# Performance work log

Measured on AMD Instinct MI355X. Metric: run time of the kernel, lower is better.

The kernel has to match this reference:

```python
import jax, jax.numpy as jnp
import numpy as np

B = 16384   # batch (agents x parallel envs)
IN = 12     # input_dim
H = 64      # hidden_dim -> 2H = 128
OUT = 25    # output_dim (forced by x[:,0:5]..x[:,20:25] slicing)


def setup_inputs() -> dict:
    key = jax.random.key(0)
    ks = jax.random.split(key, 24)
    n = lambda k, s: jax.random.normal(k, s, dtype=jnp.float32)
    s = 0.1  # scale params to keep SiLU/softmax in a sane range
    return {
        "x": n(ks[0], (B, IN)),
        "na": 4,
        # mlp_in: Linear(IN, 2H) + SiLU
        "W_in": n(ks[1], (2 * H, IN)) * s, "b_in": n(ks[2], (2 * H,)) * s,
        # first attention (2H)
        "Aq4": n(ks[3], (2 * H, 2 * H)) * s, "Bq4": n(ks[4], (2 * H,)) * s,
        "Ak4": n(ks[5], (2 * H, 2 * H)) * s, "Bk4": n(ks[6], (2 * H,)) * s,
        "Av4": n(ks[7], (2 * H, 2 * H)) * s, "Bv4": n(ks[8], (2 * H,)) * s,
        # mlp_hidden_4: Linear(2H, H) + SiLU
        "W_h": n(ks[9], (H, 2 * H)) * s, "b_h": n(ks[10], (H,)) * s,
        # second attention (H)
        "Aq7": n(ks[11], (H, H)) * s, "Bq7": n(ks[12], (H,)) * s,
        "Ak7": n(ks[13], (H, H)) * s, "Bk7": n(ks[14], (H,)) * s,
        "Av7": n(ks[15], (H, H)) * s, "Bv7": n(ks[16], (H,)) * s,
        # mlp_out: Linear(H, OUT) + SiLU
        "W_out": n(ks[17], (OUT, H)) * s, "b_out": n(ks[18], (OUT,)) * s,
    }


def _attn(h, Aq, Bq, Ak, Bk, Av, Bv):
    # h: [B, D]; torch does bmm(A, x^T)+B with x of shape [B,1,D] -> seq-len-1
    # attention, i.e. scores are an outer product q k^T of shape [B, D, D].
    q = jax.nn.silu(h @ Aq.T + Bq)                      # [B, D]
    k = jax.nn.silu(h @ Ak.T + Bk)                      # [B, D]
    v = jax.nn.silu(h @ Av.T + Bv)                      # [B, D]
    a = jax.nn.softmax(q[:, :, None] * k[:, None, :], axis=2)  # [B, D, D]
    return jax.nn.silu(jnp.einsum("bij,bj->bi", a, v))  # [B, D]


def reference(x, na, W_in, b_in, Aq4, Bq4, Ak4, Bk4, Av4, Bv4,
              W_h, b_h, Aq7, Bq7, Ak7, Bk7, Av7, Bv7, W_out, b_out):
    h = jax.nn.silu(x @ W_in.T + b_in)                  # [B, 2H]
    h = _attn(h, Aq4, Bq4, Ak4, Bk4, Av4, Bv4)          # [B, 2H]
    h = jax.nn.silu(h @ W_h.T + b_h)                    # [B, H]
    h = _attn(h, Aq7, Bq7, Ak7, Bk7, Av7, Bv7)          # [B, H]
    y = jax.nn.silu(h @ W_out.T + b_out)                # [B, 25]

    # block-diagonal quadratic-form assembly (l=2, kron with ones(1,2))
    M11 = jnp.sum(y[:, 0:5] ** 2, axis=1)               # [B]
    M12 = jnp.sum(y[:, 5:10] ** 2, axis=1)
    M21 = jnp.sum(y[:, 10:15] ** 2, axis=1)
    M22 = jnp.sum(y[:, 15:20] ** 2, axis=1)
    Mpp = jnp.sum(y[:, 20:25] ** 2, axis=1)             # [B]
    q = y[:, :4]                                        # [B, 4] = [q0,q1,q2,q3]
    # M = [[diag(M11), diag(M12)],[diag(M21), diag(M22)]] (each 2x2 diag)
    quad = (M11 * (q[:, 0] ** 2 + q[:, 1] ** 2)
            + (M12 + M21) * (q[:, 0] * q[:, 2] + q[:, 1] * q[:, 3])
            + M22 * (q[:, 2] ** 2 + q[:, 3] ** 2))
    return (quad + Mpp)[:, None]                        # [B, 1]
```

## Files before the change

### kernel.cpp

```cpp
#include <hip/hip_runtime.h>

#define RPW 4
#define WAVES 4
#define RPB (RPW * WAVES)
#define NM 14

using short8 = __attribute__((ext_vector_type(8))) short;
using f32x4  = __attribute__((ext_vector_type(4))) float;

#define LOG2E 1.4426950408889634f

static __device__ __forceinline__ float ex2(float x) { return __builtin_amdgcn_exp2f(x); }
static __device__ __forceinline__ float rcpf_(float x) { return __builtin_amdgcn_rcpf(x); }
static __device__ __forceinline__ float silu_(float x) {
    return x * rcpf_(1.0f + ex2(-x * LOG2E));
}
static __device__ __forceinline__ unsigned short bfhi(float x) {
    return (unsigned short)(__float_as_uint(x) >> 16);
}
static __device__ __forceinline__ unsigned short bfrn(float x) {
    unsigned u = __float_as_uint(x);
    return (unsigned short)((u + 0x7fffu + ((u >> 16) & 1u)) >> 16);
}
static __device__ __forceinline__ float bf2f(unsigned short h) {
    return __uint_as_float(((unsigned)h) << 16);
}

template <int CTRL>
static __device__ __forceinline__ float dpp_rot(float v) {
    return __uint_as_float(
        __builtin_amdgcn_update_dpp(0u, __float_as_uint(v), CTRL, 0xF, 0xF, true));
}
static __device__ __forceinline__ float rsum16(float v) {
    v += dpp_rot<0x128>(v);
    v += dpp_rot<0x124>(v);
    v += dpp_rot<0x122>(v);
    v += dpp_rot<0x121>(v);
    return v;
}

__constant__ float c_invfact[15] = {
    1.f, 1.f, 0.5f, 1.f/6, 1.f/24, 1.f/120, 1.f/720, 1.f/5040, 1.f/40320,
    1.f/362880, 1.f/3628800, 1.f/39916800, 1.f/479001600,
    1.f/6227020800.f, 1.f/87178291200.f};

template <int O, int I>
__device__ __forceinline__ void tr(const float* __restrict__ s, float* __restrict__ d,
                                   int t0, int stride) {
    for (int idx = t0; idx < O * I; idx += stride) {
        int o = idx / I, in = idx - o * I;
        d[in * O + o] = s[idx];
    }
}

template <int TILES, int KTS, int K>
__device__ __forceinline__ void frag_cvt(const float* __restrict__ A,
                                         unsigned short* __restrict__ dst,
                                         int t0, int stride) {
    const int total = TILES * KTS * 2 * 512;
    for (int idx = t0; idx < total; idx += stride) {
        int e = idx & 7;
        int lane = (idx >> 3) & 63;
        int h = (idx >> 9) & 1;
        int kt = (idx >> 10) % KTS;
        int tile = (idx >> 10) / KTS;
        int row = tile * 16 + (lane & 15);
        int col = kt * 32 + (lane >> 4) * 8 + e;
        float a = A[row * K + col];
        unsigned short hi = bfhi(a);
        dst[idx] = h ? bfhi(a - bf2f(hi)) : hi;
    }
}

__global__ void tweights(const float* __restrict__ s0, const float* __restrict__ s1,
                         const float* __restrict__ s2, const float* __restrict__ s3,
                         const float* __restrict__ s4, const float* __restrict__ s5,
                         const float* __restrict__ s6, const float* __restrict__ s7,
                         float* __restrict__ ws) {
    const int stride = gridDim.x * blockDim.x;
    const int t0 = blockIdx.x * blockDim.x + threadIdx.x;
    tr<128, 12>(s0, ws + 0, t0, stride);
    unsigned short* u4 = (unsigned short*)(ws + 1536);
    frag_cvt<8, 4, 128>(s1, u4 + 0,     t0, stride);
    frag_cvt<8, 4, 128>(s2, u4 + 32768, t0, stride);
    frag_cvt<8, 4, 128>(s3, u4 + 65536, t0, stride);
    unsigned short* wh = (unsigned short*)(ws + 50688);
    frag_cvt<4, 4, 128>(s4, wh, t0, stride);
    unsigned short* u7 = (unsigned short*)(ws + 58880);
    frag_cvt<4, 2, 64>(s5, u7 + 0,     t0, stride);
    frag_cvt<4, 2, 64>(s6, u7 + 8192,  t0, stride);
    frag_cvt<4, 2, 64>(s7, u7 + 16384, t0, stride);
}

__global__ __launch_bounds__(256, 4) void fused_net(
    const float* __restrict__ x, const float* __restrict__ ws,
    const float* __restrict__ b_in,
    const float* __restrict__ Bq4, const float* __restrict__ Bk4, const float* __restrict__ Bv4,
    const float* __restrict__ b_h,
    const float* __restrict__ Bq7, const float* __restrict__ Bk7, const float* __restrict__ Bv7,
    const float* __restrict__ Wout, const float* __restrict__ b_out,
    float* __restrict__ out) {
    __shared__ __align__(16) unsigned short hAhi[16][136], hAlo[16][136];
    __shared__ __align__(16) unsigned short h2hi[16][80],  h2lo[16][80];
    __shared__ __align__(16) float sQ[16][132];
    __shared__ __align__(16) unsigned short sKVb[16][132][2];
    __shared__ __align__(16) float h3T[WAVES][64][RPW];
    __shared__ __align__(16) float sXT[WAVES][12][RPW];
    __shared__ __align__(16) float sY[WAVES][RPW][26];

    const int tid = threadIdx.x;
    const int w = tid >> 6;
    const int l = tid & 63;
    const int row0 = blockIdx.x * RPB + w * RPW;
    const int m16 = l & 15, quad = l >> 4;
    const int g = l & 15, r = l >> 4;
    const int R = w * RPW + r;

    const float* WinT = ws + 0;

    float bias4[6];
    #pragma unroll
    for (int t = 0; t < 6; t++) {
        const int nt = w * 6 + t;
        const int mat = nt >> 3;
        const int n = (nt & 7) * 16 + m16;
        const float* bp = (mat == 0) ? Bq4 : (mat == 1) ? Bk4 : Bv4;
        bias4[t] = bp[n];
    }
    float biasH = b_h[w * 16 + m16];
    float bias7[3];
    #pragma unroll
    for (int t = 0; t < 3; t++) {
        const int nt = w * 3 + t;
        const int mat = nt >> 2;
        const int n = (nt & 3) * 16 + m16;
        const float* bp = (mat == 0) ? Bq7 : (mat == 1) ? Bk7 : Bv7;
        bias7[t] = bp[n];
    }

    if (l < 12 * RPW) {
        float v = x[row0 * 12 + l];
        int rr = l / 12, in = l - rr * 12;
        sXT[w][in][rr] = v;
    }

    {
        float2 bb = *(const float2*)&b_in[2 * l];
        float a0[RPW], a1[RPW];
        #pragma unroll
        for (int rr = 0; rr < RPW; rr++) { a0[rr] = bb.x; a1[rr] = bb.y; }
        #pragma unroll
        for (int in = 0; in < 12; in++) {
            float2 wv = *(const float2*)&WinT[in * 128 + 2 * l];
            float4 xr = *(const float4*)&sXT[w][in][0];
            a0[0] = fmaf(xr.x, wv.x, a0[0]); a1[0] = fmaf(xr.x, wv.y, a1[0]);
            a0[1] = fmaf(xr.y, wv.x, a0[1]); a1[1] = fmaf(xr.y, wv.y, a1[1]);
            a0[2] = fmaf(xr.z, wv.x, a0[2]); a1[2] = fmaf(xr.z, wv.y, a1[2]);
            a0[3] = fmaf(xr.w, wv.x, a0[3]); a1[3] = fmaf(xr.w, wv.y, a1[3]);
        }
        #pragma unroll
        for (int rr = 0; rr < RPW; rr++) {
            float h0 = silu_(a0[rr]), h1 = silu_(a1[rr]);
            unsigned short h0h = bfhi(h0), h1h = bfhi(h1);
            float r0 = h0 - bf2f(h0h), r1 = h1 - bf2f(h1h);
            *(unsigned*)&hAhi[w * 4 + rr][2 * l] = (unsigned)h0h | ((unsigned)h1h << 16);
            *(unsigned*)&hAlo[w * 4 + rr][2 * l] = (unsigned)bfhi(r0) | ((unsigned)bfhi(r1) << 16);
        }
    }
    __syncthreads();

    {
        short8 Ah[4], Al[4];
        #pragma unroll
        for (int kt = 0; kt < 4; kt++) {
            Ah[kt] = *(const short8*)&hAhi[m16][kt * 32 + quad * 8];
            Al[kt] = *(const short8*)&hAlo[m16][kt * 32 + quad * 8];
        }
        const unsigned short* F4 = (const unsigned short*)(ws + 1536);
        short8 cb[4][2], nb[4][2];
        auto ldt = [&](int t, short8 fr[4][2]) {
            const int nt = w * 6 + t;
            const int mat = nt >> 3, tile = nt & 7;
            const unsigned short* bp = F4 + mat * 32768 + tile * 4096 + l * 8;
            #pragma unroll
            for (int kt = 0; kt < 4; kt++) {
                fr[kt][0] = *(const short8*)(bp + kt * 1024);
                fr[kt][1] = *(const short8*)(bp + kt * 1024 + 512);
            }
        };
        ldt(0, cb);
        #pragma unroll
        for (int t = 0; t < 6; t++) {
            if (t < 5) ldt(t + 1, nb);
            f32x4 acc0 = {0.f, 0.f, 0.f, 0.f};
            f32x4 acc1 = {0.f, 0.f, 0.f, 0.f};
            #pragma unroll
            for (int kt = 0; kt < 4; kt++) {
                acc0 = __builtin_amdgcn_mfma_f32_16x16x32_bf16(Ah[kt], cb[kt][0], acc0, 0, 0, 0);
                acc1 = __builtin_amdgcn_mfma_f32_16x16x32_bf16(Ah[kt], cb[kt][1], acc1, 0, 0, 0);
                acc1 = __builtin_amdgcn_mfma_f32_16x16x32_bf16(Al[kt], cb[kt][0], acc1, 0, 0, 0);
            }
            const int nt = w * 6 + t;
            const int mat = nt >> 3;
            const int n = (nt & 7) * 16 + m16;
            const float b = bias4[t];
            #pragma unroll
            for (int reg = 0; reg < 4; reg++) {
                int row = quad * 4 + reg;
                float val = silu_(b + acc0[reg] + acc1[reg]);
                if (mat == 0)      sQ[row][n] = val;
                else if (mat == 1) sKVb[row][n][0] = bfrn(val);
                else               sKVb[row][n][1] = bfrn(val);
            }
            #pragma unroll
            for (int kt = 0; kt < 4; kt++) { cb[kt][0] = nb[kt][0]; cb[kt][1] = nb[kt][1]; }
        }
    }
    __syncthreads();

    short8 whf[4][2];
    {
        const unsigned short* bp = (const unsigned short*)(ws + 50688) + w * 4096 + l * 8;
        #pragma unroll
        for (int kt = 0; kt < 4; kt++) {
            whf[kt][0] = *(const short8*)(bp + kt * 1024);
            whf[kt][1] = *(const short8*)(bp + kt * 1024 + 512);
        }
    }
    {
        float dmom[NM];
        float nmom[NM + 1];
        #pragma unroll
        for (int m = 0; m < NM; m++) dmom[m] = 0.f;
        #pragma unroll
        for (int m = 0; m <= NM; m++) nmom[m] = 0.f;
        uint4 u0 = *(const uint4*)&sKVb[R][g * 8][0];
        uint4 u1 = *(const uint4*)&sKVb[R][g * 8 + 4][0];
        unsigned us[8] = {u0.x, u0.y, u0.z, u0.w, u1.x, u1.y, u1.z, u1.w};
        #pragma unroll
        for (int jj = 0; jj < 8; jj++) {
            unsigned u = us[jj];
            float kf = __uint_as_float(u << 16);
            float vf = __uint_as_float(u & 0xffff0000u);
            nmom[0] += vf;
            float p = kf;
            dmom[0] += p; nmom[1] = fmaf(vf, p, nmom[1]);
            #pragma unroll
            for (int m = 1; m < NM; m++) {
                p *= kf;
                dmom[m] += p;
                nmom[m + 1] = fmaf(vf, p, nmom[m + 1]);
            }
        }
        #pragma unroll
        for (int m = 0; m < NM; m++) dmom[m] = rsum16(dmom[m]);
        #pragma unroll
        for (int m = 0; m <= NM; m++) nmom[m] = rsum16(nmom[m]);
        float cd[NM + 1], cn[NM + 1];
        cd[0] = 128.f; cn[0] = nmom[0];
        #pragma unroll
        for (int m = 1; m <= NM; m++) {
            cd[m] = dmom[m - 1] * c_invfact[m];
            cn[m] = nmom[m] * c_invfact[m];
        }
        float4 qa = *(const float4*)&sQ[R][g * 8];
        float4 qb = *(const float4*)&sQ[R][g * 8 + 4];
        float qs[8] = {qa.x, qa.y, qa.z, qa.w, qb.x, qb.y, qb.z, qb.w};
        unsigned hiw[4], low[4];
        #pragma unroll
        for (int i = 0; i < 8; i++) {
            float t = qs[i];
            float d = cd[NM], nn = cn[NM];
            #pragma unroll
            for (int m = NM - 1; m >= 0; m--) {
                d = fmaf(d, t, cd[m]);
                nn = fmaf(nn, t, cn[m]);
            }
            float o = silu_(nn * rcpf_(d));
            unsigned short oh = bfhi(o);
            unsigned short olo = bfhi(o - bf2f(oh));
            if (i & 1) { hiw[i >> 1] |= ((unsigned)oh) << 16; low[i >> 1] |= ((unsigned)olo) << 16; }
            else       { hiw[i >> 1] = oh; low[i >> 1] = olo; }
        }
        *(uint4*)&hAhi[R][g * 8] = make_uint4(hiw[0], hiw[1], hiw[2], hiw[3]);
        *(uint4*)&hAlo[R][g * 8] = make_uint4(low[0], low[1], low[2], low[3]);
    }
    __syncthreads();

    short8 u7f[3][2][2];
    {
        const unsigned short* U7 = (const unsigned short*)(ws + 58880);
        #pragma unroll
        for (int t = 0; t < 3; t++) {
            const int nt = w * 3 + t;
            const int mat = nt >> 2, tile = nt & 3;
            const unsigned short* bp = U7 + mat * 8192 + tile * 2048 + l * 8;
            #pragma unroll
            for (int kt = 0; kt < 2; kt++) {
                u7f[t][kt][0] = *(const short8*)(bp + kt * 1024);
                u7f[t][kt][1] = *(const short8*)(bp + kt * 1024 + 512);
            }
        }
    }
    {
        short8 Ah[4], Al[4];
        #pragma unroll
        for (int kt = 0; kt < 4; kt++) {
            Ah[kt] = *(const short8*)&hAhi[m16][kt * 32 + quad * 8];
            Al[kt] = *(const short8*)&hAlo[m16][kt * 32 + quad * 8];
        }
        const int n = w * 16 + m16;
        f32x4 acc0 = {0.f, 0.f, 0.f, 0.f};
        f32x4 acc1 = {0.f, 0.f, 0.f, 0.f};
        #pragma unroll
        for (int kt = 0; kt < 4; kt++) {
            acc0 = __builtin_amdgcn_mfma_f32_16x16x32_bf16(Ah[kt], whf[kt][0], acc0, 0, 0, 0);
            acc1 = __builtin_amdgcn_mfma_f32_16x16x32_bf16(Ah[kt], whf[kt][1], acc1, 0, 0, 0);
            acc1 = __builtin_amdgcn_mfma_f32_16x16x32_bf16(Al[kt], whf[kt][0], acc1, 0, 0, 0);
        }
        #pragma unroll
        for (int reg = 0; reg < 4; reg++) {
            int row = quad * 4 + reg;
            float hv = silu_(biasH + acc0[reg] + acc1[reg]);
            unsigned short hh = bfhi(hv);
            h2hi[row][n] = hh;
            h2lo[row][n] = bfhi(hv - bf2f(hh));
        }
    }
    __syncthreads();

    {
        short8 Ah[2], Al[2];
        #pragma unroll
        for (int kt = 0; kt < 2; kt++) {
            Ah[kt] = *(const short8*)&h2hi[m16][kt * 32 + quad * 8];
            Al[kt] = *(const short8*)&h2lo[m16][kt * 32 + quad * 8];
        }
        #pragma unroll
        for (int t = 0; t < 3; t++) {
            const int nt = w * 3 + t;
            const int mat = nt >> 2;
            const int n = (nt & 3) * 16 + m16;
            f32x4 acc0 = {0.f, 0.f, 0.f, 0.f};
            f32x4 acc1 = {0.f, 0.f, 0.f, 0.f};
            #pragma unroll
            for (int kt = 0; kt < 2; kt++) {
                acc0 = __builtin_amdgcn_mfma_f32_16x16x32_bf16(Ah[kt], u7f[t][kt][0], acc0, 0, 0, 0);
                acc1 = __builtin_amdgcn_mfma_f32_16x16x32_bf16(Ah[kt], u7f[t][kt][1], acc1, 0, 0, 0);
                acc1 = __builtin_amdgcn_mfma_f32_16x16x32_bf16(Al[kt], u7f[t][kt][0], acc1, 0, 0, 0);
            }
            const float b = bias7[t];
            #pragma unroll
            for (int reg = 0; reg < 4; reg++) {
                int row = quad * 4 + reg;
                float val = silu_(b + acc0[reg] + acc1[reg]);
                if (mat == 0)      sQ[row][n] = val;
                else if (mat == 1) sKVb[row][n][0] = bfrn(val);
                else               sKVb[row][n][1] = bfrn(val);
            }
        }
    }
    __syncthreads();

    float4 wq[8];
    float bb7;
    {
        const int o_ = l & 31;
        const int half_ = l >> 5;
        const int oc_ = (o_ < 25) ? o_ : 0;
        const float* wp = Wout + oc_ * 64 + half_ * 32;
        #pragma unroll
        for (int q = 0; q < 8; q++) wq[q] = *(const float4*)&wp[4 * q];
        bb7 = (half_ == 0) ? b_out[oc_] : 0.f;
    }
    {
        float dmom[NM];
        float nmom[NM + 1];
        #pragma unroll
        for (int m = 0; m < NM; m++) dmom[m] = 0.f;
        #pragma unroll
        for (int m = 0; m <= NM; m++) nmom[m] = 0.f;
        uint2 u0 = *(const uint2*)&sKVb[R][g * 4][0];
        uint2 u1 = *(const uint2*)&sKVb[R][g * 4 + 2][0];
        unsigned us[4] = {u0.x, u0.y, u1.x, u1.y};
        #pragma unroll
        for (int jj = 0; jj < 4; jj++) {
            unsigned u = us[jj];
            float kf = __uint_as_float(u << 16);
            float vf = __uint_as_float(u & 0xffff0000u);
            nmom[0] += vf;
            float p = kf;
            dmom[0] += p; nmom[1] = fmaf(vf, p, nmom[1]);
            #pragma unroll
            for (int m = 1; m < NM; m++) {
                p *= kf;
                dmom[m] += p;
                nmom[m + 1] = fmaf(vf, p, nmom[m + 1]);
            }
        }
        #pragma unroll
        for (int m = 0; m < NM; m++) dmom[m] = rsum16(dmom[m]);
        #pragma unroll
        for (int m = 0; m <= NM; m++) nmom[m] = rsum16(nmom[m]);
        float cd[NM + 1], cn[NM + 1];
        cd[0] = 64.f; cn[0] = nmom[0];
        #pragma unroll
        for (int m = 1; m <= NM; m++) {
            cd[m] = dmom[m - 1] * c_invfact[m];
            cn[m] = nmom[m] * c_invfact[m];
        }
        float4 qa = *(const float4*)&sQ[R][g * 4];
        float qs[4] = {qa.x, qa.y, qa.z, qa.w};
        #pragma unroll
        for (int i = 0; i < 4; i++) {
            float t = qs[i];
            float d = cd[NM], nn = cn[NM];
            #pragma unroll
            for (int m = NM - 1; m >= 0; m--) {
                d = fmaf(d, t, cd[m]);
                nn = fmaf(nn, t, cn[m]);
            }
            h3T[w][g * 4 + i][r] = silu_(nn * rcpf_(d));
        }
    }

    {
        const int half = l >> 5;
        float y[RPW];
        #pragma unroll
        for (int rr = 0; rr < RPW; rr++) y[rr] = bb7;
        const int in0 = half * 32;
        #pragma unroll
        for (int q = 0; q < 8; q++) {
            float wa[4] = {wq[q].x, wq[q].y, wq[q].z, wq[q].w};
            #pragma unroll
            for (int ii = 0; ii < 4; ii++) {
                int in = in0 + 4 * q + ii;
                float4 xr = *(const float4*)&h3T[w][in][0];
                y[0] = fmaf(xr.x, wa[ii], y[0]);
                y[1] = fmaf(xr.y, wa[ii], y[1]);
                y[2] = fmaf(xr.z, wa[ii], y[2]);
                y[3] = fmaf(xr.w, wa[ii], y[3]);
            }
        }
        #pragma unroll
        for (int rr = 0; rr < RPW; rr++) {
            float full = y[rr] + __shfl_xor(y[rr], 32, 64);
            if (l < 25) sY[w][rr][l] = silu_(full);
        }
    }

    if (l < RPW) {
        const int rr = l;
        float y[25];
        #pragma unroll
        for (int c = 0; c < 25; c++) y[c] = sY[w][rr][c];
        float M11 = 0.f, M12 = 0.f, M21 = 0.f, M22 = 0.f, Mpp = 0.f;
        #pragma unroll
        for (int c = 0; c < 5; c++) {
            M11 = fmaf(y[c], y[c], M11);
            M12 = fmaf(y[5 + c], y[5 + c], M12);
            M21 = fmaf(y[10 + c], y[10 + c], M21);
            M22 = fmaf(y[15 + c], y[15 + c], M22);
            Mpp = fmaf(y[20 + c], y[20 + c], Mpp);
        }
        float quad = M11 * (y[0] * y[0] + y[1] * y[1])
                   + (M12 + M21) * (y[0] * y[2] + y[1] * y[3])
                   + M22 * (y[2] * y[2] + y[3] * y[3]);
        out[row0 + rr] = quad + Mpp;
    }
}

extern "C" void kernel_launch(void* const* d_in, const int* in_sizes, int n_in,
                              void* d_out, int out_size, void* d_ws, size_t ws_size,
                              hipStream_t stream) {
    const float* x    = (const float*)d_in[0];
    const float* W_in = (const float*)d_in[2];
    const float* b_in = (const float*)d_in[3];
    const float* Aq4  = (const float*)d_in[4];
    const float* Bq4  = (const float*)d_in[5];
    const float* Ak4  = (const float*)d_in[6];
    const float* Bk4  = (const float*)d_in[7];
    const float* Av4  = (const float*)d_in[8];
    const float* Bv4  = (const float*)d_in[9];
    const float* W_h  = (const float*)d_in[10];
    const float* b_h  = (const float*)d_in[11];
    const float* Aq7  = (const float*)d_in[12];
    const float* Bq7  = (const float*)d_in[13];
    const float* Ak7  = (const float*)d_in[14];
    const float* Bk7  = (const float*)d_in[15];
    const float* Av7  = (const float*)d_in[16];
    const float* Bv7  = (const float*)d_in[17];
    const float* Wout = (const float*)d_in[18];
    const float* bout = (const float*)d_in[19];
    float* ws = (float*)d_ws;

    tweights<<<256, 256, 0, stream>>>(W_in, Aq4, Ak4, Av4, W_h, Aq7, Ak7, Av7, ws);

    const int B = in_sizes[0] / 12;
    const int grid = B / RPB;
    fused_net<<<grid, 256, 0, stream>>>(x, ws, b_in, Bq4, Bk4, Bv4,
                                        b_h, Bq7, Bk7, Bv7, Wout, bout, (float*)d_out);
}
```

Measured before the change: 132.6 us.

## Make each wave compute its own rows end-to-end, removing block barriers

Each wave now runs every MFMA tile for its own 4 rows, replicated into a 16-row A fragment, so no other wave's output is needed and all __syncthreads are removed. This repeats the weight-fragment loads and MFMA work about 4x per wave, with 12 of the 16 MFMA rows wasted, and only lane quad 0 writes results. Biases are folded into the accumulator init. A hashed s_sleep stagger at the start spreads out waves' global loads. Bias and Wout values are now loaded inside the loops instead of being prefetched into registers.

```diff
diff --git a/kernel.cpp b/kernel.cpp
--- a/kernel.cpp
+++ b/kernel.cpp
@@ -52,7 +52,6 @@
         d[in * O + o] = s[idx];
     }
 }
-
 template <int TILES, int KTS, int K>
 __device__ __forceinline__ void frag_cvt(const float* __restrict__ A,
                                          unsigned short* __restrict__ dst,
@@ -113,29 +112,19 @@
     const int l = tid & 63;
     const int row0 = blockIdx.x * RPB + w * RPW;
     const int m16 = l & 15, quad = l >> 4;
+    const int m4 = m16 & 3;
     const int g = l & 15, r = l >> 4;
     const int R = w * RPW + r;
 
     const float* WinT = ws + 0;
-
-    float bias4[6];
-    #pragma unroll
-    for (int t = 0; t < 6; t++) {
-        const int nt = w * 6 + t;
-        const int mat = nt >> 3;
-        const int n = (nt & 7) * 16 + m16;
-        const float* bp = (mat == 0) ? Bq4 : (mat == 1) ? Bk4 : Bv4;
-        bias4[t] = bp[n];
-    }
-    float biasH = b_h[w * 16 + m16];
-    float bias7[3];
-    #pragma unroll
-    for (int t = 0; t < 3; t++) {
-        const int nt = w * 3 + t;
-        const int mat = nt >> 2;
-        const int n = (nt & 3) * 16 + m16;
-        const float* bp = (mat == 0) ? Bq7 : (mat == 1) ? Bk7 : Bv7;
-        bias7[t] = bp[n];
+    const unsigned short* F4 = (const unsigned short*)(ws + 1536);
+    const unsigned short* WH = (const unsigned short*)(ws + 50688);
+    const unsigned short* U7 = (const unsigned short*)(ws + 58880);
+
+    {
+        unsigned hsh = (blockIdx.x * 2654435761u) >> 27;
+        int stag = (int)((hsh ^ (unsigned)w) & 7u);
+        for (int i = 0; i < stag; i++) __builtin_amdgcn_s_sleep(8);
     }
 
     if (l < 12 * RPW) {
@@ -167,66 +156,45 @@
             *(unsigned*)&hAlo[w * 4 + rr][2 * l] = (unsigned)bfhi(r0) | ((unsigned)bfhi(r1) << 16);
         }
     }
-    __syncthreads();
 
     {
         short8 Ah[4], Al[4];
         #pragma unroll
         for (int kt = 0; kt < 4; kt++) {
-            Ah[kt] = *(const short8*)&hAhi[m16][kt * 32 + quad * 8];
-            Al[kt] = *(const short8*)&hAlo[m16][kt * 32 + quad * 8];
-        }
-        const unsigned short* F4 = (const unsigned short*)(ws + 1536);
-        short8 cb[4][2], nb[4][2];
-        auto ldt = [&](int t, short8 fr[4][2]) {
-            const int nt = w * 6 + t;
+            Ah[kt] = *(const short8*)&hAhi[w * 4 + m4][kt * 32 + quad * 8];
+            Al[kt] = *(const short8*)&hAlo[w * 4 + m4][kt * 32 + quad * 8];
+        }
+        #pragma unroll 2
+        for (int nt = 0; nt < 24; nt++) {
             const int mat = nt >> 3, tile = nt & 7;
-            const unsigned short* bp = F4 + mat * 32768 + tile * 4096 + l * 8;
+            const int n = tile * 16 + m16;
+            const float* bp = (mat == 0) ? Bq4 : (mat == 1) ? Bk4 : Bv4;
+            const float b = bp[n];
+            f32x4 acc0 = {b, b, b, b};
+            f32x4 acc1 = {0.f, 0.f, 0.f, 0.f};
+            f32x4 acc2 = {0.f, 0.f, 0.f, 0.f};
+            const unsigned short* bq = F4 + mat * 32768 + tile * 4096 + l * 8;
             #pragma unroll
             for (int kt = 0; kt < 4; kt++) {
-                fr[kt][0] = *(const short8*)(bp + kt * 1024);
-                fr[kt][1] = *(const short8*)(bp + kt * 1024 + 512);
-            }
-        };
-        ldt(0, cb);
-        #pragma unroll
-        for (int t = 0; t < 6; t++) {
-            if (t < 5) ldt(t + 1, nb);
-            f32x4 acc0 = {0.f, 0.f, 0.f, 0.f};
-            f32x4 acc1 = {0.f, 0.f, 0.f, 0.f};
-            #pragma unroll
-            for (int kt = 0; kt < 4; kt++) {
-                acc0 = __builtin_amdgcn_mfma_f32_16x16x32_bf16(Ah[kt], cb[kt][0], acc0, 0, 0, 0);
-                acc1 = __builtin_amdgcn_mfma_f32_16x16x32_bf16(Ah[kt], cb[kt][1], acc1, 0, 0, 0);
-                acc1 = __builtin_amdgcn_mfma_f32_16x16x32_bf16(Al[kt], cb[kt][0], acc1, 0, 0, 0);
-            }
-            const int nt = w * 6 + t;
-            const int mat = nt >> 3;
-            const int n = (nt & 7) * 16 + m16;
-            const float b = bias4[t];
-            #pragma unroll
-            for (int reg = 0; reg < 4; reg++) {
-                int row = quad * 4 + reg;
-                float val = silu_(b + acc0[reg] + acc1[reg]);
-                if (mat == 0)      sQ[row][n] = val;
-                else if (mat == 1) sKVb[row][n][0] = bfrn(val);
-                else               sKVb[row][n][1] = bfrn(val);
-            }
-            #pragma unroll
-            for (int kt = 0; kt < 4; kt++) { cb[kt][0] = nb[kt][0]; cb[kt][1] = nb[kt][1]; }
-        }
-    }
-    __syncthreads();
-
-    short8 whf[4][2];
-    {
-        const unsigned short* bp = (const unsigned short*)(ws + 50688) + w * 4096 + l * 8;
-        #pragma unroll
-        for (int kt = 0; kt < 4; kt++) {
-            whf[kt][0] = *(const short8*)(bp + kt * 1024);
-            whf[kt][1] = *(const short8*)(bp + kt * 1024 + 512);
-        }
-    }
+                short8 bh = *(const short8*)(bq + kt * 1024);
+                short8 bl = *(const short8*)(bq + kt * 1024 + 512);
+                acc0 = __builtin_amdgcn_mfma_f32_16x16x32_bf16(Ah[kt], bh, acc0, 0, 0, 0);
+                acc1 = __builtin_amdgcn_mfma_f32_16x16x32_bf16(Ah[kt], bl, acc1, 0, 0, 0);
+                acc2 = __builtin_amdgcn_mfma_f32_16x16x32_bf16(Al[kt], bh, acc2, 0, 0, 0);
+            }
+            if (quad == 0) {
+                #pragma unroll
+                for (int reg = 0; reg < 4; reg++) {
+                    int row = w * 4 + reg;
+                    float val = silu_(acc0[reg] + acc1[reg] + acc2[reg]);
+                    if (mat == 0)      sQ[row][n] = val;
+                    else if (mat == 1) sKVb[row][n][0] = bfrn(val);
+                    else               sKVb[row][n][1] = bfrn(val);
+                }
+            }
+        }
+    }
+
     {
         float dmom[NM];
         float nmom[NM + 1];
@@ -285,94 +253,81 @@
         *(uint4*)&hAhi[R][g * 8] = make_uint4(hiw[0], hiw[1], hiw[2], hiw[3]);
         *(uint4*)&hAlo[R][g * 8] = make_uint4(low[0], low[1], low[2], low[3]);
     }
-    __syncthreads();
-
-    short8 u7f[3][2][2];
-    {
-        const unsigned short* U7 = (const unsigned short*)(ws + 58880);
-        #pragma unroll
-        for (int t = 0; t < 3; t++) {
-            const int nt = w * 3 + t;
+
+    {
+        short8 Ah[4], Al[4];
+        #pragma unroll
+        for (int kt = 0; kt < 4; kt++) {
+            Ah[kt] = *(const short8*)&hAhi[w * 4 + m4][kt * 32 + quad * 8];
+            Al[kt] = *(const short8*)&hAlo[w * 4 + m4][kt * 32 + quad * 8];
+        }
+        #pragma unroll 2
+        for (int t = 0; t < 4; t++) {
+            const int n = t * 16 + m16;
+            const float b = b_h[n];
+            f32x4 acc0 = {b, b, b, b};
+            f32x4 acc1 = {0.f, 0.f, 0.f, 0.f};
+            f32x4 acc2 = {0.f, 0.f, 0.f, 0.f};
+            const unsigned short* bq = WH + t * 4096 + l * 8;
+            #pragma unroll
+            for (int kt = 0; kt < 4; kt++) {
+                short8 bh = *(const short8*)(bq + kt * 1024);
+                short8 bl = *(const short8*)(bq + kt * 1024 + 512);
+                acc0 = __builtin_amdgcn_mfma_f32_16x16x32_bf16(Ah[kt], bh, acc0, 0, 0, 0);
+                acc1 = __builtin_amdgcn_mfma_f32_16x16x32_bf16(Ah[kt], bl, acc1, 0, 0, 0);
+                acc2 = __builtin_amdgcn_mfma_f32_16x16x32_bf16(Al[kt], bh, acc2, 0, 0, 0);
+            }
+            if (quad == 0) {
+                #pragma unroll
+                for (int reg = 0; reg < 4; reg++) {
+                    int row = w * 4 + reg;
+                    float hv = silu_(acc0[reg] + acc1[reg] + acc2[reg]);
+                    unsigned short hh = bfhi(hv);
+                    h2hi[row][n] = hh;
+                    h2lo[row][n] = bfhi(hv - bf2f(hh));
+                }
+            }
+        }
+    }
+
+    {
+        short8 Ah[2], Al[2];
+        #pragma unroll
+        for (int kt = 0; kt < 2; kt++) {
+            Ah[kt] = *(const short8*)&h2hi[w * 4 + m4][kt * 32 + quad * 8];
+            Al[kt] = *(const short8*)&h2lo[w * 4 + m4][kt * 32 + quad * 8];
+        }
+        #pragma unroll 2
+        for (int nt = 0; nt < 12; nt++) {
             const int mat = nt >> 2, tile = nt & 3;
-            const unsigned short* bp = U7 + mat * 8192 + tile * 2048 + l * 8;
+            const int n = tile * 16 + m16;
+            const float* bp = (mat == 0) ? Bq7 : (mat == 1) ? Bk7 : Bv7;
+            const float b = bp[n];
+            f32x4 acc0 = {b, b, b, b};
+            f32x4 acc1 = {0.f, 0.f, 0.f, 0.f};
+            f32x4 acc2 = {0.f, 0.f, 0.f, 0.f};
+            const unsigned short* bq = U7 + mat * 8192 + tile * 2048 + l * 8;
             #pragma unroll
             for (int kt = 0; kt < 2; kt++) {
-                u7f[t][kt][0] = *(const short8*)(bp + kt * 1024);
-                u7f[t][kt][1] = *(const short8*)(bp + kt * 1024 + 512);
-            }
-        }
-    }
-    {
-        short8 Ah[4], Al[4];
-        #pragma unroll
-        for (int kt = 0; kt < 4; kt++) {
-            Ah[kt] = *(const short8*)&hAhi[m16][kt * 32 + quad * 8];
-            Al[kt] = *(const short8*)&hAlo[m16][kt * 32 + quad * 8];
-        }
-        const int n = w * 16 + m16;
-        f32x4 acc0 = {0.f, 0.f, 0.f, 0.f};
-        f32x4 acc1 = {0.f, 0.f, 0.f, 0.f};
-        #pragma unroll
-        for (int kt = 0; kt < 4; kt++) {
-            acc0 = __builtin_amdgcn_mfma_f32_16x16x32_bf16(Ah[kt], whf[kt][0], acc0, 0, 0, 0);
-            acc1 = __builtin_amdgcn_mfma_f32_16x16x32_bf16(Ah[kt], whf[kt][1], acc1, 0, 0, 0);
-            acc1 = __builtin_amdgcn_mfma_f32_16x16x32_bf16(Al[kt], whf[kt][0], acc1, 0, 0, 0);
-        }
-        #pragma unroll
-        for (int reg = 0; reg < 4; reg++) {
-            int row = quad * 4 + reg;
-            float hv = silu_(biasH + acc0[reg] + acc1[reg]);
-            unsigned short hh = bfhi(hv);
-            h2hi[row][n] = hh;
-            h2lo[row][n] = bfhi(hv - bf2f(hh));
-        }
-    }
-    __syncthreads();
-
-    {
-        short8 Ah[2], Al[2];
-        #pragma unroll
-        for (int kt = 0; kt < 2; kt++) {
-            Ah[kt] = *(const short8*)&h2hi[m16][kt * 32 + quad * 8];
-            Al[kt] = *(const short8*)&h2lo[m16][kt * 32 + quad * 8];
-        }
-        #pragma unroll
-        for (int t = 0; t < 3; t++) {
-            const int nt = w * 3 + t;
-            const int mat = nt >> 2;
-            const int n = (nt & 3) * 16 + m16;
-            f32x4 acc0 = {0.f, 0.f, 0.f, 0.f};
-            f32x4 acc1 = {0.f, 0.f, 0.f, 0.f};
-            #pragma unroll
-            for (int kt = 0; kt < 2; kt++) {
-                acc0 = __builtin_amdgcn_mfma_f32_16x16x32_bf16(Ah[kt], u7f[t][kt][0], acc0, 0, 0, 0);
-                acc1 = __builtin_amdgcn_mfma_f32_16x16x32_bf16(Ah[kt], u7f[t][kt][1], acc1, 0, 0, 0);
-                acc1 = __builtin_amdgcn_mfma_f32_16x16x32_bf16(Al[kt], u7f[t][kt][0], acc1, 0, 0, 0);
-            }
-            const float b = bias7[t];
-            #pragma unroll
-            for (int reg = 0; reg < 4; reg++) {
-                int row = quad * 4 + reg;
-                float val = silu_(b + acc0[reg] + acc1[reg]);
-                if (mat == 0)      sQ[row][n] = val;
-                else if (mat == 1) sKVb[row][n][0] = bfrn(val);
-                else               sKVb[row][n][1] = bfrn(val);
-            }
-        }
-    }
-    __syncthreads();
-
-    float4 wq[8];
-    float bb7;
-    {
-        const int o_ = l & 31;
-        const int half_ = l >> 5;
-        const int oc_ = (o_ < 25) ? o_ : 0;
-        const float* wp = Wout + oc_ * 64 + half_ * 32;
-        #pragma unroll
-        for (int q = 0; q < 8; q++) wq[q] = *(const float4*)&wp[4 * q];
-        bb7 = (half_ == 0) ? b_out[oc_] : 0.f;
-    }
+                short8 bh = *(const short8*)(bq + kt * 1024);
+                short8 bl = *(const short8*)(bq + kt * 1024 + 512);
+                acc0 = __builtin_amdgcn_mfma_f32_16x16x32_bf16(Ah[kt], bh, acc0, 0, 0, 0);
+                acc1 = __builtin_amdgcn_mfma_f32_16x16x32_bf16(Ah[kt], bl, acc1, 0, 0, 0);
+                acc2 = __builtin_amdgcn_mfma_f32_16x16x32_bf16(Al[kt], bh, acc2, 0, 0, 0);
+            }
+            if (quad == 0) {
+                #pragma unroll
+                for (int reg = 0; reg < 4; reg++) {
+                    int row = w * 4 + reg;
+                    float val = silu_(acc0[reg] + acc1[reg] + acc2[reg]);
+                    if (mat == 0)      sQ[row][n] = val;
+                    else if (mat == 1) sKVb[row][n][0] = bfrn(val);
+                    else               sKVb[row][n][1] = bfrn(val);
+                }
+            }
+        }
+    }
+
     {
         float dmom[NM];
         float nmom[NM + 1];
@@ -425,14 +380,19 @@
     }
 
     {
+        const int o = l & 31;
         const int half = l >> 5;
+        const int oc = (o < 25) ? o : 0;
         float y[RPW];
-        #pragma unroll
-        for (int rr = 0; rr < RPW; rr++) y[rr] = bb7;
+        float bb = (half == 0) ? b_out[oc] : 0.f;
+        #pragma unroll
+        for (int rr = 0; rr < RPW; rr++) y[rr] = bb;
         const int in0 = half * 32;
+        const float* wp = Wout + oc * 64 + in0;
         #pragma unroll
         for (int q = 0; q < 8; q++) {
-            float wa[4] = {wq[q].x, wq[q].y, wq[q].z, wq[q].w};
+            float4 wq = *(const float4*)&wp[4 * q];
+            float wa[4] = {wq.x, wq.y, wq.z, wq.w};
             #pragma unroll
             for (int ii = 0; ii < 4; ii++) {
                 int in = in0 + 4 * q + ii;
@@ -464,10 +424,10 @@
             M22 = fmaf(y[15 + c], y[15 + c], M22);
             Mpp = fmaf(y[20 + c], y[20 + c], Mpp);
         }
-        float quad = M11 * (y[0] * y[0] + y[1] * y[1])
-                   + (M12 + M21) * (y[0] * y[2] + y[1] * y[3])
-                   + M22 * (y[2] * y[2] + y[3] * y[3]);
-        out[row0 + rr] = quad + Mpp;
+        float quad_ = M11 * (y[0] * y[0] + y[1] * y[1])
+                    + (M12 + M21) * (y[0] * y[2] + y[1] * y[3])
+                    + M22 * (y[2] * y[2] + y[3] * y[3]);
+        out[row0 + rr] = quad_ + Mpp;
     }
 }
 
```

Measured after the change: 168.2 us. 1.27x slower.
